# Kernel optimization log

Measured on AMD Instinct MI355X. Metric: run time of the kernel, lower is better.

## Reference

```python
import jax, jax.numpy as jnp
import numpy as np

B, L1, L, DIM_IN, DIM_H, DIM_M = 8, 64, 1024, 512, 512, 512


def setup_inputs() -> dict:
    key = jax.random.key(0)
    ks = jax.random.split(key, 7)
    return {
        "query": jax.random.normal(ks[0], (L1, DIM_H), dtype=jnp.float32),
        "keys": jax.random.normal(ks[1], (B, L, DIM_IN), dtype=jnp.float32),
        "values": jax.random.normal(ks[2], (B, L, DIM_IN), dtype=jnp.float32),
        # nn.Linear weights: Wx (dim_middle, dim_in) no bias; Wh (dim_middle, dim_h) with bias; w (dim_middle,) no bias
        "Wx": jax.random.normal(ks[3], (DIM_M, DIM_IN), dtype=jnp.float32) * 0.02,
        "Wh": jax.random.normal(ks[4], (DIM_M, DIM_H), dtype=jnp.float32) * 0.02,
        "bh": jax.random.normal(ks[5], (DIM_M,), dtype=jnp.float32) * 0.02,
        "w": jax.random.normal(ks[6], (DIM_M,), dtype=jnp.float32) * 0.02,
    }


def reference(query, keys, values, Wx, Wh, bh, w):
    # mode='concept': query [l1, dh], keys/values [b, l, d]
    kx = jnp.einsum('bld,md->blm', keys, Wx)          # [b, l, m]
    qh = jnp.einsum('qd,md->qm', query, Wh) + bh       # [l1, m]
    g = jax.nn.relu(kx[:, None, :, :] + qh[None, :, None, :])  # [b, l1, l, m]
    scores = jnp.einsum('bqlm,m->bql', g, w)           # [b, l1, l]
    e = jax.nn.softmax(scores, axis=-1)                # softmax over key len (dim 2)
    return jnp.einsum('bql,bld->bqd', e, values)       # [b, l1, dv]
```

## Files before the change

### kernel.cpp

```cpp
#include <hip/hip_runtime.h>
#include <hip/hip_bf16.h>

#define BB 8
#define L1 64
#define LL 1024
#define DD 512

typedef float f32x4 __attribute__((ext_vector_type(4)));
typedef _Float16 f16;
typedef _Float16 f16x2 __attribute__((ext_vector_type(2)));
typedef _Float16 f16x4 __attribute__((ext_vector_type(4)));
typedef _Float16 f16x8 __attribute__((ext_vector_type(8)));

union F16x8u { f16x8 v; f16x2 h[4]; };

__global__ __launch_bounds__(256) void kxqh_kernel(
    const float* __restrict__ keys,
    const float* __restrict__ query,
    const float* __restrict__ Wx,
    const float* __restrict__ Wh,
    const float* __restrict__ bh,
    f16* __restrict__ kx,
    f16* __restrict__ qh) {
  __shared__ char lds[49152] __attribute__((aligned(128)));
  const int t = threadIdx.x;
  const int lane = t & 63;
  const int w = t >> 6;
  const int fq = lane >> 4, fr = lane & 15;
  const int bid = blockIdx.x;

  if (bid < 8) {
    const int m0 = bid * 64;
    const int wid = w;
    f32x4 acc[4] = {};
    float4 rq[4], rw[4];
#define LOADQ(KC)                                                              \
    do {                                                                       \
      _Pragma("unroll") for (int i = 0; i < 4; ++i) {                          \
        int slot = t + i * 256;                                                \
        int row = slot >> 4, c4 = (slot & 15) * 4;                             \
        rq[i] = *reinterpret_cast<const float4*>(query + (size_t)row * DD + (KC)*64 + c4); \
        rw[i] = *reinterpret_cast<const float4*>(Wh + (size_t)(m0 + row) * DD + (KC)*64 + c4); \
      }                                                                        \
    } while (0)
    LOADQ(0);
    for (int kc = 0; kc < 8; ++kc) {
      #pragma unroll
      for (int i = 0; i < 4; ++i) {
        int slot = t + i * 256;
        int row = slot >> 4, c4 = (slot & 15) * 4;
        f16x4 hq, hw;
        hq[0] = (f16)rq[i].x; hq[1] = (f16)rq[i].y; hq[2] = (f16)rq[i].z; hq[3] = (f16)rq[i].w;
        hw[0] = (f16)rw[i].x; hw[1] = (f16)rw[i].y; hw[2] = (f16)rw[i].z; hw[3] = (f16)rw[i].w;
        *reinterpret_cast<f16x4*>(lds + row * 144 + c4 * 2) = hq;
        *reinterpret_cast<f16x4*>(lds + 9216 + row * 144 + c4 * 2) = hw;
      }
      if (kc < 7) LOADQ(kc + 1);
      __syncthreads();
      #pragma unroll
      for (int kh = 0; kh < 2; ++kh) {
        f16x8 bf = *reinterpret_cast<const f16x8*>(
            lds + 9216 + (wid * 16 + fr) * 144 + kh * 64 + fq * 16);
        #pragma unroll
        for (int qf = 0; qf < 4; ++qf) {
          f16x8 af = *reinterpret_cast<const f16x8*>(
              lds + (qf * 16 + fr) * 144 + kh * 64 + fq * 16);
          acc[qf] = __builtin_amdgcn_mfma_f32_16x16x32_f16(af, bf, acc[qf], 0, 0, 0);
        }
      }
      __syncthreads();
    }
#undef LOADQ
    #pragma unroll
    for (int qf = 0; qf < 4; ++qf) {
      int m = m0 + wid * 16 + fr;
      float bias = bh[m];
      #pragma unroll
      for (int r = 0; r < 4; ++r)
        qh[(size_t)(qf * 16 + fq * 4 + r) * DD + m] = (f16)(acc[qf][r] + bias);
    }
    return;
  }

  const int kb = bid - 8;
  const int rt = kb & 127;
  const int mt = kb >> 7;
  const int rowA0 = rt * 64;
  const int m0 = mt * 128;
  const int wr = w >> 1, wc = w & 1;

  f32x4 acc[2][4] = {};
  float4 ra[4], rb[8];

#define LOADK(K0)                                                              \
  do {                                                                         \
    _Pragma("unroll") for (int i = 0; i < 4; ++i) {                            \
      int flat = t * 4 + i * 1024;                                             \
      int row = flat >> 6, col = flat & 63;                                    \
      ra[i] = *reinterpret_cast<const float4*>(keys + (size_t)(rowA0 + row) * DD + (K0) + col); \
    }                                                                          \
    _Pragma("unroll") for (int i = 0; i < 8; ++i) {                            \
      int flat = t * 4 + i * 1024;                                             \
      int row = flat >> 6, col = flat & 63;                                    \
      rb[i] = *reinterpret_cast<const float4*>(Wx + (size_t)(m0 + row) * DD + (K0) + col); \
    }                                                                          \
  } while (0)

  LOADK(0);
  for (int s = 0; s < 8; ++s) {
    const int base = (s & 1) * 24576;
    #pragma unroll
    for (int i = 0; i < 4; ++i) {
      int flat = t * 4 + i * 1024;
      int row = flat >> 6, col = flat & 63;
      f16x4 ha;
      ha[0] = (f16)ra[i].x; ha[1] = (f16)ra[i].y; ha[2] = (f16)ra[i].z; ha[3] = (f16)ra[i].w;
      *reinterpret_cast<f16x4*>(lds + base + row * 128 + ((col * 2) ^ ((row & 7) << 4))) = ha;
    }
    #pragma unroll
    for (int i = 0; i < 8; ++i) {
      int flat = t * 4 + i * 1024;
      int row = flat >> 6, col = flat & 63;
      f16x4 hb;
      hb[0] = (f16)rb[i].x; hb[1] = (f16)rb[i].y; hb[2] = (f16)rb[i].z; hb[3] = (f16)rb[i].w;
      *reinterpret_cast<f16x4*>(lds + base + 8192 + row * 128 + ((col * 2) ^ ((row & 7) << 4))) = hb;
    }
    if (s < 7) LOADK((s + 1) * 64);
    __syncthreads();
    #pragma unroll
    for (int kh = 0; kh < 2; ++kh) {
      f16x8 af[2], bf[4];
      #pragma unroll
      for (int mi = 0; mi < 2; ++mi) {
        int row = wr * 32 + mi * 16 + fr;
        af[mi] = *reinterpret_cast<const f16x8*>(
            lds + base + row * 128 + ((kh * 64 + fq * 16) ^ ((row & 7) << 4)));
      }
      #pragma unroll
      for (int ni = 0; ni < 4; ++ni) {
        int row = wc * 64 + ni * 16 + fr;
        bf[ni] = *reinterpret_cast<const f16x8*>(
            lds + base + 8192 + row * 128 + ((kh * 64 + fq * 16) ^ ((row & 7) << 4)));
      }
      #pragma unroll
      for (int mi = 0; mi < 2; ++mi)
        #pragma unroll
        for (int ni = 0; ni < 4; ++ni)
          acc[mi][ni] = __builtin_amdgcn_mfma_f32_16x16x32_f16(
              af[mi], bf[ni], acc[mi][ni], 0, 0, 0);
    }
  }
#undef LOADK
  #pragma unroll
  for (int mi = 0; mi < 2; ++mi) {
    #pragma unroll
    for (int ni = 0; ni < 4; ++ni) {
      int row = rowA0 + wr * 32 + mi * 16 + fq * 4;
      int col = m0 + wc * 64 + ni * 16 + fr;
      #pragma unroll
      for (int r = 0; r < 4; ++r)
        kx[(size_t)(row + r) * DD + col] = (f16)acc[mi][ni][r];
    }
  }
}

__global__ __launch_bounds__(512) void score5_kernel(
    const f16* __restrict__ kx,
    const f16* __restrict__ qh,
    const float* __restrict__ w,
    float* __restrict__ sc,
    float* __restrict__ pmax) {
  const int b = blockIdx.x & 7;
  const int l0 = (blockIdx.x >> 3) * 32;
  const int t = threadIdx.x;
  __shared__ __align__(16) f16 kxs[32][136];
  __shared__ __align__(16) f16 qhs[64][136];
  __shared__ __align__(16) f16 wsf[DD];
  __shared__ float smax[64][17];
  if (t < 128) {
    float4 wv = *reinterpret_cast<const float4*>(w + t * 4);
    f16x4 hv; hv[0] = (f16)wv.x; hv[1] = (f16)wv.y; hv[2] = (f16)wv.z; hv[3] = (f16)wv.w;
    *reinterpret_cast<f16x4*>(&wsf[t * 4]) = hv;
  }
  const int qb = t & 31;
  const int lp = t >> 5;
  float acc[2][2] = {};
  uint4 rkx, rqh[2];

#define LOADM(M0)                                                              \
  do {                                                                         \
    {                                                                          \
      int row = t >> 4, col = (t & 15) * 8;                                    \
      rkx = *reinterpret_cast<const uint4*>(kx + (size_t)(b * LL + l0 + row) * DD + (M0) + col); \
    }                                                                          \
    _Pragma("unroll") for (int p = 0; p < 2; ++p) {                            \
      int slot = t + p * 512;                                                  \
      int row = slot >> 4, col = (slot & 15) * 8;                              \
      rqh[p] = *reinterpret_cast<const uint4*>(qh + (size_t)row * DD + (M0) + col); \
    }                                                                          \
  } while (0)

  LOADM(0);
  for (int m0 = 0; m0 < DD; m0 += 128) {
    {
      int row = t >> 4, col = (t & 15) * 8;
      *reinterpret_cast<uint4*>(&kxs[row][col]) = rkx;
    }
    #pragma unroll
    for (int p = 0; p < 2; ++p) {
      int slot = t + p * 512;
      int row = slot >> 4, col = (slot & 15) * 8;
      *reinterpret_cast<uint4*>(&qhs[row][col]) = rqh[p];
    }
    if (m0 < DD - 128) LOADM(m0 + 128);
    __syncthreads();
    #pragma unroll 2
    for (int mm = 0; mm < 128; mm += 8) {
      F16x8u kv0, kv1, wv;
      kv0.v = *reinterpret_cast<const f16x8*>(&kxs[lp * 2][mm]);
      kv1.v = *reinterpret_cast<const f16x8*>(&kxs[lp * 2 + 1][mm]);
      wv.v = *reinterpret_cast<const f16x8*>(&wsf[m0 + mm]);
      #pragma unroll
      for (int j = 0; j < 2; ++j) {
        F16x8u qv, g0, g1;
        qv.v = *reinterpret_cast<const f16x8*>(&qhs[qb + 32 * j][mm]);
        f16x8 zz = {};
        g0.v = __builtin_elementwise_max(kv0.v + qv.v, zz);
        g1.v = __builtin_elementwise_max(kv1.v + qv.v, zz);
        #pragma unroll
        for (int c = 0; c < 4; ++c) {
          acc[0][j] = __builtin_amdgcn_fdot2(g0.h[c], wv.h[c], acc[0][j], false);
          acc[1][j] = __builtin_amdgcn_fdot2(g1.h[c], wv.h[c], acc[1][j], false);
        }
      }
    }
    __syncthreads();
  }
#undef LOADM
  #pragma unroll
  for (int i = 0; i < 2; ++i)
    #pragma unroll
    for (int j = 0; j < 2; ++j)
      sc[((size_t)b * L1 + qb + 32 * j) * LL + l0 + lp * 2 + i] = acc[i][j];
  #pragma unroll
  for (int j = 0; j < 2; ++j)
    smax[qb + 32 * j][lp] = fmaxf(acc[0][j], acc[1][j]);
  __syncthreads();
  if (t < 64) {
    float m = smax[t][0];
    #pragma unroll
    for (int i = 1; i < 16; ++i) m = fmaxf(m, smax[t][i]);
    pmax[((size_t)b * L1 + t) * 32 + (l0 >> 5)] = m;
  }
}

__global__ __launch_bounds__(512) void fso2_kernel(
    const float* __restrict__ sc,
    const float* __restrict__ pmax,
    const float* __restrict__ v,
    float* __restrict__ out) {
  __shared__ __align__(16) char es[64 * 256];
  __shared__ __align__(16) char vt[16 * 256];
  __shared__ float rowm[64];
  __shared__ float rowinv[64];
  __shared__ float spart[64][17];
  __shared__ f32x4 accbuf[4][64];
  const int t = threadIdx.x;
  const int lane = t & 63;
  const int w = t >> 6;
  const int fq = lane >> 4, fr = lane & 15;
  const int bid = blockIdx.x;
  const int b = bid & 7;
  const int d0 = (bid >> 3) * 16;
  const float* scb = sc + (size_t)b * L1 * LL;
  const float* vb = v + (size_t)b * LL * DD;

  const int r0 = t >> 4;
  const int r1 = (t + 512) >> 4;
  const int ec8 = t & 15;
  const int vl = t >> 2;
  const int dq = (t & 3) * 4;
  float4 rsc[2][2];
  float4 rv;

#define LOADC(LC)                                                              \
  do {                                                                         \
    const float* s0 = scb + (size_t)r0 * LL + (LC) * 128 + ec8 * 8;            \
    rsc[0][0] = *reinterpret_cast<const float4*>(s0);                          \
    rsc[0][1] = *reinterpret_cast<const float4*>(s0 + 4);                      \
    const float* s1 = scb + (size_t)r1 * LL + (LC) * 128 + ec8 * 8;            \
    rsc[1][0] = *reinterpret_cast<const float4*>(s1);                          \
    rsc[1][1] = *reinterpret_cast<const float4*>(s1 + 4);                      \
    rv = *reinterpret_cast<const float4*>(                                     \
        vb + (size_t)((LC) * 128 + vl) * DD + d0 + dq);                        \
  } while (0)

  LOADC(0);
  if (t < 64) {
    const float* pm = pmax + ((size_t)b * L1 + t) * 32;
    float4 m4 = *reinterpret_cast<const float4*>(pm);
    #pragma unroll
    for (int i = 1; i < 8; ++i) {
      float4 x = *reinterpret_cast<const float4*>(pm + i * 4);
      m4.x = fmaxf(m4.x, x.x); m4.y = fmaxf(m4.y, x.y);
      m4.z = fmaxf(m4.z, x.z); m4.w = fmaxf(m4.w, x.w);
    }
    rowm[t] = fmaxf(fmaxf(m4.x, m4.y), fmaxf(m4.z, m4.w));
  }
  __syncthreads();
  float rmv[2] = {rowm[r0], rowm[r1]};
  float spp[2] = {0.f, 0.f};
  f32x4 acc = {};
  const int qs = (w & 3) * 16;
  const int ksh = (w >> 2) * 2;

  for (int c = 0; c < 8; ++c) {
    #pragma unroll
    for (int p = 0; p < 2; ++p) {
      int q = p ? r1 : r0;
      float xs[8] = {rsc[p][0].x, rsc[p][0].y, rsc[p][0].z, rsc[p][0].w,
                     rsc[p][1].x, rsc[p][1].y, rsc[p][1].z, rsc[p][1].w};
      f16x8 h;
      #pragma unroll
      for (int j = 0; j < 8; ++j) {
        float e = __expf(xs[j] - rmv[p]);
        spp[p] += e;
        h[j] = (f16)e;
      }
      int byte = q * 256 + ((ec8 * 16) ^ ((q & 7) << 4));
      *reinterpret_cast<f16x8*>(es + byte) = h;
    }
    {
      float vs[4] = {rv.x, rv.y, rv.z, rv.w};
      #pragma unroll
      for (int j = 0; j < 4; ++j) {
        int d = dq + j;
        int byte = d * 256 + ((2 * vl) ^ ((d & 7) << 4));
        *reinterpret_cast<f16*>(vt + byte) = (f16)vs[j];
      }
    }
    if (c < 7) LOADC(c + 1);
    __syncthreads();
    #pragma unroll
    for (int ki = 0; ki < 2; ++ki) {
      int ks = ksh + ki;
      int qa = qs + fr;
      int colb = ks * 64 + fq * 16;
      f16x8 a = *reinterpret_cast<const f16x8*>(es + qa * 256 + (colb ^ ((qa & 7) << 4)));
      f16x8 bb = *reinterpret_cast<const f16x8*>(vt + fr * 256 + (colb ^ ((fr & 7) << 4)));
      acc = __builtin_amdgcn_mfma_f32_16x16x32_f16(a, bb, acc, 0, 0, 0);
    }
    __syncthreads();
  }
#undef LOADC
  spart[r0][ec8] = spp[0];
  spart[r1][ec8] = spp[1];
  if (w >= 4) accbuf[w & 3][lane] = acc;
  __syncthreads();
  if (t < 64) {
    float S = 0.f;
    #pragma unroll
    for (int i = 0; i < 16; ++i) S += spart[t][i];
    rowinv[t] = 1.f / S;
  }
  __syncthreads();
  if (w < 4) {
    f32x4 ah = accbuf[w][lane];
    acc += ah;
    #pragma unroll
    for (int r = 0; r < 4; ++r) {
      int q = qs + fq * 4 + r;
      out[((size_t)b * L1 + q) * DD + d0 + fr] = acc[r] * rowinv[q];
    }
  }
}

extern "C" void kernel_launch(void* const* d_in, const int* in_sizes, int n_in,
                              void* d_out, int out_size, void* d_ws, size_t ws_size,
                              hipStream_t stream) {
  const float* query  = (const float*)d_in[0];
  const float* keys   = (const float*)d_in[1];
  const float* values = (const float*)d_in[2];
  const float* Wx     = (const float*)d_in[3];
  const float* Wh     = (const float*)d_in[4];
  const float* bh     = (const float*)d_in[5];
  const float* w      = (const float*)d_in[6];
  float* out = (float*)d_out;

  char* ws = (char*)d_ws;
  f16*   kx   = (f16*)ws;
  f16*   qh   = (f16*)(ws + 8388608);
  float* sc   = (float*)(ws + 8454144);
  float* pmax = (float*)(ws + 10551296);

  kxqh_kernel<<<520, 256, 0, stream>>>(keys, query, Wx, Wh, bh, kx, qh);
  score5_kernel<<<256, 512, 0, stream>>>(kx, qh, w, sc, pmax);
  fso2_kernel<<<256, 512, 0, stream>>>(sc, pmax, values, out);
}
```

Baseline: 49.16 us.

## Pre-convert keys and Wx to fp16, stage kx GEMM tiles via global_load_lds

The kx GEMM is split out of the combined kernel. A new pass first converts keys and Wx from fp32 to fp16 into workspace buffers, running in the same launch as the qh projection. The new kx kernel then double-buffers fp16 tiles into LDS with direct global-to-LDS loads, removing register staging and the convert-and-store work from the GEMM loop. In exchange it adds an extra kernel launch and a full write-and-reread of an fp16 copy of keys, and the qh path gets fewer blocks' worth of co-scheduling.

```diff
diff --git a/kernel.cpp b/kernel.cpp
--- a/kernel.cpp
+++ b/kernel.cpp
@@ -14,24 +14,24 @@
 
 union F16x8u { f16x8 v; f16x2 h[4]; };
 
-__global__ __launch_bounds__(256) void kxqh_kernel(
-    const float* __restrict__ keys,
+__global__ __launch_bounds__(256) void convqh_kernel(
     const float* __restrict__ query,
-    const float* __restrict__ Wx,
     const float* __restrict__ Wh,
     const float* __restrict__ bh,
-    f16* __restrict__ kx,
-    f16* __restrict__ qh) {
-  __shared__ char lds[49152] __attribute__((aligned(128)));
+    const float* __restrict__ keys,
+    const float* __restrict__ Wx,
+    f16* __restrict__ qh,
+    f16* __restrict__ keys16,
+    f16* __restrict__ wx16) {
   const int t = threadIdx.x;
-  const int lane = t & 63;
-  const int w = t >> 6;
-  const int fq = lane >> 4, fr = lane & 15;
   const int bid = blockIdx.x;
 
   if (bid < 8) {
+    __shared__ char lds[18432] __attribute__((aligned(128)));
+    const int lane = t & 63;
+    const int wid = t >> 6;
+    const int fq = lane >> 4, fr = lane & 15;
     const int m0 = bid * 64;
-    const int wid = w;
     f32x4 acc[4] = {};
     float4 rq[4], rw[4];
 #define LOADQ(KC)                                                              \
@@ -82,51 +82,68 @@
     return;
   }
 
-  const int kb = bid - 8;
-  const int rt = kb & 127;
-  const int mt = kb >> 7;
+  const int cid = bid - 8;
+  const int NK = (BB * LL * DD) / 4;
+  const int NT = NK + (DD * DD) / 4;
+  for (int i = cid * 256 + t; i < NT; i += 504 * 256) {
+    float4 v;
+    if (i < NK) v = reinterpret_cast<const float4*>(keys)[i];
+    else        v = reinterpret_cast<const float4*>(Wx)[i - NK];
+    f16x4 h;
+    h[0] = (f16)v.x; h[1] = (f16)v.y; h[2] = (f16)v.z; h[3] = (f16)v.w;
+    if (i < NK) *reinterpret_cast<f16x4*>(keys16 + (size_t)i * 4) = h;
+    else        *reinterpret_cast<f16x4*>(wx16 + (size_t)(i - NK) * 4) = h;
+  }
+}
+
+__global__ __launch_bounds__(256) void kx_kernel(
+    const f16* __restrict__ keys16,
+    const f16* __restrict__ wx16,
+    f16* __restrict__ kx) {
+  __shared__ char lds[49152] __attribute__((aligned(128)));
+  const int t = threadIdx.x;
+  const int lane = t & 63;
+  const int w = t >> 6;
+  const int wr = w >> 1, wc = w & 1;
+  const int fq = lane >> 4, fr = lane & 15;
+  const int rt = blockIdx.x & 127;
+  const int mt = blockIdx.x >> 7;
   const int rowA0 = rt * 64;
   const int m0 = mt * 128;
-  const int wr = w >> 1, wc = w & 1;
+
+  const int lrow8 = lane >> 3;
+  const int lcol = (((lane & 7) ^ lrow8) << 4) >> 1;
 
   f32x4 acc[2][4] = {};
-  float4 ra[4], rb[8];
-
-#define LOADK(K0)                                                              \
+
+#define STAGE(BUF, K0)                                                         \
   do {                                                                         \
-    _Pragma("unroll") for (int i = 0; i < 4; ++i) {                            \
-      int flat = t * 4 + i * 1024;                                             \
-      int row = flat >> 6, col = flat & 63;                                    \
-      ra[i] = *reinterpret_cast<const float4*>(keys + (size_t)(rowA0 + row) * DD + (K0) + col); \
-    }                                                                          \
-    _Pragma("unroll") for (int i = 0; i < 8; ++i) {                            \
-      int flat = t * 4 + i * 1024;                                             \
-      int row = flat >> 6, col = flat & 63;                                    \
-      rb[i] = *reinterpret_cast<const float4*>(Wx + (size_t)(m0 + row) * DD + (K0) + col); \
+    _Pragma("unroll") for (int i = 0; i < 6; ++i) {                            \
+      int c = w * 6 + i;                                                       \
+      if (c < 8) {                                                             \
+        int row = c * 8 + lrow8;                                               \
+        const f16* g = keys16 + (size_t)(rowA0 + row) * DD + (K0) + lcol;      \
+        __builtin_amdgcn_global_load_lds(                                      \
+            (const __attribute__((address_space(1))) void*)g,                  \
+            (__attribute__((address_space(3))) void*)(lds + (BUF) + c * 1024), \
+            16, 0, 0);                                                         \
+      } else {                                                                 \
+        int cb = c - 8;                                                        \
+        int row = cb * 8 + lrow8;                                              \
+        const f16* g = wx16 + (size_t)(m0 + row) * DD + (K0) + lcol;           \
+        __builtin_amdgcn_global_load_lds(                                      \
+            (const __attribute__((address_space(1))) void*)g,                  \
+            (__attribute__((address_space(3))) void*)(lds + (BUF) + 8192 + cb * 1024), \
+            16, 0, 0);                                                         \
+      }                                                                        \
     }                                                                          \
   } while (0)
 
-  LOADK(0);
+  STAGE(0, 0);
+  __syncthreads();
   for (int s = 0; s < 8; ++s) {
-    const int base = (s & 1) * 24576;
-    #pragma unroll
-    for (int i = 0; i < 4; ++i) {
-      int flat = t * 4 + i * 1024;
-      int row = flat >> 6, col = flat & 63;
-      f16x4 ha;
-      ha[0] = (f16)ra[i].x; ha[1] = (f16)ra[i].y; ha[2] = (f16)ra[i].z; ha[3] = (f16)ra[i].w;
-      *reinterpret_cast<f16x4*>(lds + base + row * 128 + ((col * 2) ^ ((row & 7) << 4))) = ha;
-    }
-    #pragma unroll
-    for (int i = 0; i < 8; ++i) {
-      int flat = t * 4 + i * 1024;
-      int row = flat >> 6, col = flat & 63;
-      f16x4 hb;
-      hb[0] = (f16)rb[i].x; hb[1] = (f16)rb[i].y; hb[2] = (f16)rb[i].z; hb[3] = (f16)rb[i].w;
-      *reinterpret_cast<f16x4*>(lds + base + 8192 + row * 128 + ((col * 2) ^ ((row & 7) << 4))) = hb;
-    }
-    if (s < 7) LOADK((s + 1) * 64);
-    __syncthreads();
+    const int cur = (s & 1) * 24576;
+    if (s < 7) STAGE(24576 - cur, (s + 1) * 64);
     #pragma unroll
     for (int kh = 0; kh < 2; ++kh) {
       f16x8 af[2], bf[4];
@@ -134,13 +151,13 @@
       for (int mi = 0; mi < 2; ++mi) {
         int row = wr * 32 + mi * 16 + fr;
         af[mi] = *reinterpret_cast<const f16x8*>(
-            lds + base + row * 128 + ((kh * 64 + fq * 16) ^ ((row & 7) << 4)));
+            lds + cur + row * 128 + ((kh * 64 + fq * 16) ^ ((row & 7) << 4)));
       }
       #pragma unroll
       for (int ni = 0; ni < 4; ++ni) {
         int row = wc * 64 + ni * 16 + fr;
         bf[ni] = *reinterpret_cast<const f16x8*>(
-            lds + base + 8192 + row * 128 + ((kh * 64 + fq * 16) ^ ((row & 7) << 4)));
+            lds + cur + 8192 + row * 128 + ((kh * 64 + fq * 16) ^ ((row & 7) << 4)));
       }
       #pragma unroll
       for (int mi = 0; mi < 2; ++mi)
@@ -149,8 +166,9 @@
           acc[mi][ni] = __builtin_amdgcn_mfma_f32_16x16x32_f16(
               af[mi], bf[ni], acc[mi][ni], 0, 0, 0);
     }
-  }
-#undef LOADK
+    __syncthreads();
+  }
+#undef STAGE
   #pragma unroll
   for (int mi = 0; mi < 2; ++mi) {
     #pragma unroll
@@ -388,12 +406,15 @@
   float* out = (float*)d_out;
 
   char* ws = (char*)d_ws;
-  f16*   kx   = (f16*)ws;
-  f16*   qh   = (f16*)(ws + 8388608);
-  float* sc   = (float*)(ws + 8454144);
-  float* pmax = (float*)(ws + 10551296);
-
-  kxqh_kernel<<<520, 256, 0, stream>>>(keys, query, Wx, Wh, bh, kx, qh);
+  f16*   kx     = (f16*)ws;
+  f16*   qh     = (f16*)(ws + 8388608);
+  float* sc     = (float*)(ws + 8454144);
+  float* pmax   = (float*)(ws + 10551296);
+  f16*   keys16 = (f16*)(ws + 10616832);
+  f16*   wx16   = (f16*)(ws + 19005440);
+
+  convqh_kernel<<<512, 256, 0, stream>>>(query, Wh, bh, keys, Wx, qh, keys16, wx16);
+  kx_kernel<<<512, 256, 0, stream>>>(keys16, wx16, kx);
   score5_kernel<<<256, 512, 0, stream>>>(kx, qh, w, sc, pmax);
   fso2_kernel<<<256, 512, 0, stream>>>(sc, pmax, values, out);
 }
```

New measurement: 51.35 us. 4.5% more time.
